# Kernel optimization log

Measured on AMD Instinct MI355X. Metric: run time of the kernel, lower is better.

Reference implementation:

```python
import jax, jax.numpy as jnp
import numpy as np

S, B, R, H, TOP, CHL = 512, 32, 8, 128, 3, 19
I = CHL + 1  # GRU input size after null-channel concat


def setup_inputs() -> dict:
    key = jax.random.key(0)
    ks = jax.random.split(key, 12)
    f = lambda k, shp, sc=0.05: jax.random.normal(k, shp, dtype=jnp.float32) * sc
    return {
        "x": f(ks[0], (B, CHL, S), 1.0),
        "Wih": f(ks[1], (R, 3 * H, I)),      # per-rim GRU input weights (torch order r,z,n)
        "Whh": f(ks[2], (R, 3 * H, H)),      # per-rim GRU hidden weights
        "Qir_w": f(ks[3], (H, H)),
        "Qir_b": f(ks[4], (H,)),
        "Kir_w": f(ks[5], (H, S)),
        "Vir_w": f(ks[6], (H, S)),
        "Qrr_w": f(ks[7], (H, H)),
        "Krr_w": f(ks[8], (H, H)),
        "Vrr_w": f(ks[9], (H, H)),
    }


def reference(x, Wih, Whh, Qir_w, Qir_b, Kir_w, Vir_w, Qrr_w, Krr_w, Vrr_w):
    Bn = x.shape[0]
    # prepend null channel, reshape to (S, B, I)
    xc = jnp.concatenate([jnp.zeros((Bn, 1, x.shape[2]), x.dtype), x], axis=1)
    xs = jnp.transpose(xc, (2, 0, 1))  # (S, B, I)

    # ---- per-rim GRU (no bias), torch gate order (r, z, n) ----
    x_proj = jnp.einsum('sbi,rgi->srbg', xs, Wih)  # (S, R, B, 3H)

    def step(hprev, xp):
        hp = jnp.einsum('rbh,rgh->rbg', hprev, Whh)
        xr, xz, xn = jnp.split(xp, 3, axis=-1)
        hr, hz, hn = jnp.split(hp, 3, axis=-1)
        r = jax.nn.sigmoid(xr + hr)
        z = jax.nn.sigmoid(xz + hz)
        n = jnp.tanh(xn + r * hn)
        hnew = (1.0 - z) * n + z * hprev
        return hnew, hnew

    h0 = jnp.zeros((R, Bn, H), x.dtype)
    _, hs = jax.lax.scan(step, h0, x_proj)      # (S, R, B, H)
    h = jnp.transpose(hs, (1, 0, 2, 3))          # (R, S, B, H)

    # ---- stage one: input attention + rim competition ----
    x_bis = jnp.transpose(xs, (1, 2, 0))         # (B, I, S)
    q = jnp.einsum('rsbh,oh->rsbo', h, Qir_w) + Qir_b
    k = jnp.einsum('bis,os->bio', x_bis, Kir_w)
    v = jnp.einsum('bis,os->bio', x_bis, Vir_w)
    qk = jnp.einsum('rsbh,bih->sbri', q, k) / (H ** 0.5)
    soft = jax.nn.softmax(qk, axis=3)            # (S, B, R, I)
    idx = jax.lax.top_k(-soft[..., 0], TOP)[1]   # (S, B, TOP)
    mask = jnp.sum(jax.nn.one_hot(idx, R, dtype=jnp.float32), axis=-2)[..., None]  # (S,B,R,1)
    mask = jax.lax.stop_gradient(mask)
    qkv = jnp.einsum('sbri,bih->sbrh', soft, v)  # (S, B, R, H)

    # NoGrad: forward identity, backward grad*mask
    h1 = qkv * mask + jax.lax.stop_gradient(qkv * (1.0 - mask))

    # ---- stage two: rim-rim attention, masked ----
    q2 = jnp.einsum('sbrh,oh->sbro', h1, Qrr_w)
    k2 = jnp.einsum('sbrh,oh->sbro', h1, Krr_w)
    v2 = jnp.einsum('sbrh,oh->sbro', h1, Vrr_w)
    qk2 = jnp.einsum('sbrh,sbch->sbrc', q2, k2)  # (S, B, R, R), no scaling (as in source)
    soft2 = jax.nn.softmax(qk2, axis=3) * mask
    out = h1 + jnp.einsum('sbrc,sbch->sbrh', soft2, v2)
    return out * mask
```

## Files before the change

### kernel.cpp

```cpp
#include <hip/hip_runtime.h>
#include <math.h>


typedef float v2f __attribute__((ext_vector_type(2)));
__device__ __forceinline__ v2f pkfma(v2f a, v2f b, v2f c) {
    return __builtin_elementwise_fma(a, b, c);
}

__global__ void kT(const float* __restrict__ Kir, const float* __restrict__ Vir,
                   const float* __restrict__ Vrr,
                   float* __restrict__ KirT, float* __restrict__ VirT,
                   float* __restrict__ VrrT) {
    int idx = blockIdx.x * 256 + threadIdx.x;
    if (idx < 65536) {
        int s = idx >> 7, o = idx & 127;
        KirT[idx] = Kir[o * 512 + s];
    } else if (idx < 131072) {
        int j = idx - 65536;
        int s = j >> 7, o = j & 127;
        VirT[j] = Vir[o * 512 + s];
    } else if (idx < 147456) {
        int j = idx - 131072;
        int g = j >> 7, h = j & 127;
        VrrT[j] = Vrr[h * 128 + g];
    }
}

__global__ __launch_bounds__(128) void kKV(const float* __restrict__ x,
        const float* __restrict__ KirT, const float* __restrict__ VirT,
        float* __restrict__ kbuf, float* __restrict__ vbuf) {
    const int b = blockIdx.x / 20, i = blockIdx.x % 20;
    const int o = threadIdx.x;
    if (i == 0) {
        kbuf[(b * 20) * 128 + o] = 0.0f;
        vbuf[(b * 20) * 128 + o] = 0.0f;
        return;
    }
    __shared__ float xL[512];
    for (int idx = threadIdx.x; idx < 512; idx += 128)
        xL[idx] = x[(b * 19 + (i - 1)) * 512 + idx];
    __syncthreads();
    float ak = 0.0f, av = 0.0f;
#pragma unroll 4
    for (int s = 0; s < 512; ++s) {
        float xv = xL[s];
        ak += xv * KirT[s * 128 + o];
        av += xv * VirT[s * 128 + o];
    }
    kbuf[(b * 20 + i) * 128 + o] = ak;
    vbuf[(b * 20 + i) * 128 + o] = av;
}

__global__ __launch_bounds__(128) void kKQ(const float* __restrict__ kbuf,
        const float* __restrict__ Qir, const float* __restrict__ Qib,
        float* __restrict__ KQ, float* __restrict__ cb) {
    const int b = blockIdx.x / 20, i = blockIdx.x % 20;
    const int h = threadIdx.x;
    __shared__ float kL[128];
    kL[h] = kbuf[(b * 20 + i) * 128 + h];
    __syncthreads();
    float acc = 0.0f;
#pragma unroll 4
    for (int o = 0; o < 128; ++o) acc += kL[o] * Qir[o * 128 + h];
    KQ[(b * 20 + i) * 128 + h] = acc;
    if (h == 0) {
        float c = 0.0f;
        for (int o = 0; o < 128; ++o) c += kL[o] * Qib[o];
        cb[b * 20 + i] = c;
    }
}

__global__ __launch_bounds__(256) void kM(const float* __restrict__ Qrr,
        const float* __restrict__ Krr, float* __restrict__ M) {
    const int h = blockIdx.x * 2 + (threadIdx.x >> 7);
    const int g = threadIdx.x & 127;
    float acc = 0.0f;
#pragma unroll 4
    for (int o = 0; o < 128; ++o) acc += Qrr[o * 128 + h] * Krr[o * 128 + g];
    M[h * 128 + g] = acc;
}

template<int CTRL>
__device__ __forceinline__ float dppadd(float v) {
    int r = __builtin_amdgcn_update_dpp(0, __float_as_int(v), CTRL, 0xF, 0xF, true);
    return v + __int_as_float(r);
}

__global__ __launch_bounds__(512, 2) void kGRU(const float* __restrict__ x,
        const float* __restrict__ Wih, const float* __restrict__ Whh,
        float* __restrict__ hs) {
    const int r = blockIdx.x >> 5;
    const int b = blockIdx.x & 31;
    const int t = threadIdx.x;
    const int j = t >> 2;
    const int kq = t & 3;

    __shared__ __align__(16) float xT[512 * 20];
    __shared__ __align__(16) float hsBuf[64 * 144];

    for (int idx = t; idx < 19 * 512; idx += 512) {
        int c = idx >> 9, s = idx & 511;
        xT[s * 20 + c] = x[(b * 19 + c) * 512 + s];
    }
    if (t < 144) hsBuf[63 * 144 + t] = 0.0f;

    v2f w0[16], w1[16], w2[16];
    {
        const float* Wb = Whh + (r * 384) * 128 + kq * 32;
        const float4* s0p = (const float4*)(Wb + (j) * 128);
        const float4* s1p = (const float4*)(Wb + (j + 128) * 128);
        const float4* s2p = (const float4*)(Wb + (j + 256) * 128);
#pragma unroll
        for (int u = 0; u < 8; ++u) {
            float4 a = s0p[u];
            w0[2*u]   = (v2f){a.x, a.y};
            w0[2*u+1] = (v2f){a.z, a.w};
            float4 bb = s1p[u];
            w1[2*u]   = (v2f){bb.x, bb.y};
            w1[2*u+1] = (v2f){bb.z, bb.w};
            float4 cc = s2p[u];
            w2[2*u]   = (v2f){cc.x, cc.y};
            w2[2*u+1] = (v2f){cc.z, cc.w};
        }
    }
    v2f wiv[9];
    float wlast;
    if (kq < 3) {
        const float* W = Wih + (r * 384 + (j + 128 * kq)) * 20;
#pragma unroll
        for (int c = 0; c < 9; ++c) wiv[c] = (v2f){W[2*c + 1], W[2*c + 2]};
        wlast = W[19];
    } else {
#pragma unroll
        for (int c = 0; c < 9; ++c) wiv[c] = (v2f){0.0f, 0.0f};
        wlast = 0.0f;
    }
    __syncthreads();

    const int jmap = j + ((j >> 5) << 2);
    const int cellBase = (b * 8 + r) * 128;
    float hprev = 0.0f;

    for (int s = 0; s < 512; ++s) {
        const int rowR = (s + 63) & 63;
        const float4* hp4 = (const float4*)(hsBuf + rowR * 144 + kq * 36);
        float4 hv[8];
#pragma unroll
        for (int u = 0; u < 8; ++u) hv[u] = hp4[u];

        v2f a0 = {0.0f, 0.0f}, a1 = {0.0f, 0.0f}, a2 = {0.0f, 0.0f};
#pragma unroll
        for (int u = 0; u < 8; ++u) {
            float4 h4 = hv[u];
            v2f hl = (v2f){h4.x, h4.y};
            v2f hh = (v2f){h4.z, h4.w};
            a0 = pkfma(w0[2*u], hl, a0); a0 = pkfma(w0[2*u+1], hh, a0);
            a1 = pkfma(w1[2*u], hl, a1); a1 = pkfma(w1[2*u+1], hh, a1);
            a2 = pkfma(w2[2*u], hl, a2); a2 = pkfma(w2[2*u+1], hh, a2);
        }
        float p0 = a0.x + a0.y;
        float p1 = a1.x + a1.y;
        float p2 = a2.x + a2.y;

        float xp;
        {
            const float4* xp4 = (const float4*)(xT + s * 20);
            float4 xa = xp4[0], xb = xp4[1], xc = xp4[2], xd = xp4[3], xe = xp4[4];
            v2f xacc = {0.0f, 0.0f};
            xacc = pkfma(wiv[0], (v2f){xa.x, xa.y}, xacc);
            xacc = pkfma(wiv[1], (v2f){xa.z, xa.w}, xacc);
            xacc = pkfma(wiv[2], (v2f){xb.x, xb.y}, xacc);
            xacc = pkfma(wiv[3], (v2f){xb.z, xb.w}, xacc);
            xacc = pkfma(wiv[4], (v2f){xc.x, xc.y}, xacc);
            xacc = pkfma(wiv[5], (v2f){xc.z, xc.w}, xacc);
            xacc = pkfma(wiv[6], (v2f){xd.x, xd.y}, xacc);
            xacc = pkfma(wiv[7], (v2f){xd.z, xd.w}, xacc);
            xacc = pkfma(wiv[8], (v2f){xe.x, xe.y}, xacc);
            xp = xacc.x + xacc.y + wlast * xe.z;
        }
        p0 += (kq == 0) ? xp : 0.0f;
        p1 += (kq == 1) ? xp : 0.0f;
        float p3 = (kq == 2) ? xp : 0.0f;

        p0 = dppadd<0xB1>(p0); p0 = dppadd<0x4E>(p0);
        p1 = dppadd<0xB1>(p1); p1 = dppadd<0x4E>(p1);
        p2 = dppadd<0xB1>(p2); p2 = dppadd<0x4E>(p2);
        p3 = dppadd<0xB1>(p3); p3 = dppadd<0x4E>(p3);

        float rg = __builtin_amdgcn_rcpf(1.0f + __expf(-p0));
        float zg = __builtin_amdgcn_rcpf(1.0f + __expf(-p1));
        float a  = p3 + rg * p2;
        float ng = 1.0f - 2.0f * __builtin_amdgcn_rcpf(__expf(2.0f * a) + 1.0f);
        float hnew = ng + zg * (hprev - ng);
        hprev = hnew;
        if (kq == 0) hsBuf[(s & 63) * 144 + jmap] = hnew;
        __syncthreads();

        if ((s & 63) == 63) {
            const int sBase = s - 63;
            const int c4 = (t & 31) * 4;
            const int cm = c4 + ((c4 >> 5) << 2);
#pragma unroll
            for (int w = 0; w < 4; ++w) {
                int rr = (t >> 5) + w * 16;
                float4 v = *(const float4*)(hsBuf + rr * 144 + cm);
                *(float4*)(hs + (size_t)(sBase + rr) * 32768 + cellBase + c4) = v;
            }
            __syncthreads();
        }
    }
}

__global__ __launch_bounds__(256) void kS1(const float* __restrict__ hs,
        const float* __restrict__ KQ, const float* __restrict__ cb,
        const float* __restrict__ vbuf,
        float* __restrict__ h1, int* __restrict__ widx, float* __restrict__ out) {
    const int b = blockIdx.x & 31;
    const int s0 = (blockIdx.x >> 5) * 16;
    const int t = threadIdx.x;
    __shared__ float KQL[20 * 132];
    __shared__ float vL[20 * 128];
    __shared__ float cbL[20];
    __shared__ float hLt[8 * 132];
    __shared__ float qkL[8 * 20];
    __shared__ float sfL[8 * 20];
    __shared__ float s0L[8];
    __shared__ int wselL[3];

    for (int idx = t; idx < 2560; idx += 256) {
        int i = idx >> 7, h = idx & 127;
        KQL[i * 132 + h] = KQ[(b * 20 + i) * 128 + h];
        vL[i * 128 + h] = vbuf[(b * 20 + i) * 128 + h];
    }
    if (t < 20) cbL[t] = cb[b * 20 + t];
    __syncthreads();

    for (int p = 0; p < 16; ++p) {
        const int s = s0 + p;
        for (int idx = t; idx < 1024; idx += 256) {
            int r = idx >> 7, h = idx & 127;
            hLt[r * 132 + h] = hs[((s * 32 + b) * 8 + r) * 128 + h];
        }
        __syncthreads();
        if (t < 152) {
            int r = t / 19, i = t % 19 + 1;
            const float* hr = &hLt[r * 132];
            const float* kg = &KQL[i * 132];
            float a = 0.0f;
#pragma unroll 4
            for (int h = 0; h < 128; ++h) a += hr[h] * kg[h];
            qkL[r * 20 + i] = (a + cbL[i]) * 0.08838834764831845f;
        }
        if (t < 8) qkL[t * 20] = 0.0f;
        __syncthreads();
        if (t < 8) {
            float m = -3.4e38f;
            for (int i = 0; i < 20; ++i) m = fmaxf(m, qkL[t * 20 + i]);
            float sum = 0.0f;
            for (int i = 0; i < 20; ++i) {
                float e = expf(qkL[t * 20 + i] - m);
                sfL[t * 20 + i] = e;
                sum += e;
            }
            float inv = 1.0f / sum;
            for (int i = 0; i < 20; ++i) sfL[t * 20 + i] *= inv;
            s0L[t] = sfL[t * 20];
        }
        __syncthreads();
        if (t == 0) {
            unsigned chosen = 0;
            for (int n = 0; n < 3; ++n) {
                float best = 3.4e38f; int bi = 0;
                for (int r2 = 0; r2 < 8; ++r2) {
                    if (chosen & (1u << r2)) continue;
                    float v = s0L[r2];
                    if (v < best) { best = v; bi = r2; }
                }
                chosen |= (1u << bi);
                wselL[n] = bi;
                widx[(s * 32 + b) * 3 + n] = bi;
            }
        }
        __syncthreads();
        {
            const int h = t & 127, rq = t >> 7;
            float a0 = 0, a1 = 0, a2 = 0, a3 = 0;
            for (int i = 1; i < 20; ++i) {
                float vv = vL[i * 128 + h];
                a0 += sfL[(rq * 4 + 0) * 20 + i] * vv;
                a1 += sfL[(rq * 4 + 1) * 20 + i] * vv;
                a2 += sfL[(rq * 4 + 2) * 20 + i] * vv;
                a3 += sfL[(rq * 4 + 3) * 20 + i] * vv;
            }
            const int pairBase = (s * 32 + b) * 8;
            float av[4] = {a0, a1, a2, a3};
#pragma unroll
            for (int jj = 0; jj < 4; ++jj) {
                int rim = rq * 4 + jj;
                h1[(pairBase + rim) * 128 + h] = av[jj];
                bool win = (wselL[0] == rim) || (wselL[1] == rim) || (wselL[2] == rim);
                if (!win) out[(pairBase + rim) * 128 + h] = 0.0f;
            }
        }
        __syncthreads();
    }
}

template<int EPI>
__global__ __launch_bounds__(256) void kGemm(
        const float* __restrict__ Asrc,
        const float* __restrict__ Bm,
        const int* __restrict__ widx,
        const float* __restrict__ h1g,
        float* __restrict__ C) {
    __shared__ float ALt[64][132];
    __shared__ float BL[64][128];
    const int n0 = blockIdx.x * 128;
    const int t = threadIdx.x;
    const int tr = t >> 4, tc = t & 15;
    const int q0 = 2 * tc, q1 = 2 * tc + 1;
    const int bq0 = (q0 ^ (q0 >> 3)) * 4;
    const int bq1 = (q1 ^ (q1 >> 3)) * 4;
    float acc[8][8];
#pragma unroll
    for (int i = 0; i < 8; ++i)
#pragma unroll
        for (int jj = 0; jj < 8; ++jj) acc[i][jj] = 0.0f;

    for (int kc = 0; kc < 128; kc += 64) {
        __syncthreads();
#pragma unroll
        for (int i = 0; i < 8; ++i) {
            int idx = t + i * 256;
            int row = idx >> 4, qk = idx & 15;
            const float* src;
            if (EPI == 0) {
                int n = n0 + row;
                int pair = n / 3;
                int rim = widx[n];
                src = Asrc + ((pair << 3) + rim) * 128 + kc + qk * 4;
            } else {
                src = Asrc + (n0 + row) * 128 + kc + qk * 4;
            }
            float4 a = *(const float4*)src;
            ALt[qk * 4 + 0][row] = a.x;
            ALt[qk * 4 + 1][row] = a.y;
            ALt[qk * 4 + 2][row] = a.z;
            ALt[qk * 4 + 3][row] = a.w;
        }
#pragma unroll
        for (int i = 0; i < 8; ++i) {
            int idx = t + i * 256;
            int kk = idx >> 5, qc = idx & 31;
            float4 bv = *(const float4*)(Bm + (kc + kk) * 128 + qc * 4);
            int pos = (qc ^ (qc >> 3)) * 4;
            *(float4*)&BL[kk][pos] = bv;
        }
        __syncthreads();
#pragma unroll 2
        for (int k = 0; k < 64; ++k) {
            float4 a0 = *(const float4*)&ALt[k][8 * tr];
            float4 a1 = *(const float4*)&ALt[k][8 * tr + 4];
            float4 b0 = *(const float4*)&BL[k][bq0];
            float4 b1 = *(const float4*)&BL[k][bq1];
            float ar[8] = {a0.x, a0.y, a0.z, a0.w, a1.x, a1.y, a1.z, a1.w};
            float bc[8] = {b0.x, b0.y, b0.z, b0.w, b1.x, b1.y, b1.z, b1.w};
#pragma unroll
            for (int i = 0; i < 8; ++i)
#pragma unroll
                for (int jj = 0; jj < 8; ++jj) acc[i][jj] += ar[i] * bc[jj];
        }
    }
    if (EPI == 0) {
#pragma unroll
        for (int i = 0; i < 8; ++i) {
            int row = n0 + 8 * tr + i;
            *(float4*)(C + row * 128 + 8 * tc) =
                make_float4(acc[i][0], acc[i][1], acc[i][2], acc[i][3]);
            *(float4*)(C + row * 128 + 8 * tc + 4) =
                make_float4(acc[i][4], acc[i][5], acc[i][6], acc[i][7]);
        }
    } else {
#pragma unroll
        for (int i = 0; i < 8; ++i) {
            int n = n0 + 8 * tr + i;
            int pair = n / 3;
            int rim = widx[n];
            int base = ((pair << 3) + rim) * 128 + 8 * tc;
            float4 w0 = *(const float4*)(h1g + base);
            float4 w1 = *(const float4*)(h1g + base + 4);
            *(float4*)(C + base) = make_float4(acc[i][0] + w0.x, acc[i][1] + w0.y,
                                               acc[i][2] + w0.z, acc[i][3] + w0.w);
            *(float4*)(C + base + 4) = make_float4(acc[i][4] + w1.x, acc[i][5] + w1.y,
                                                   acc[i][6] + w1.z, acc[i][7] + w1.w);
        }
    }
}

__global__ __launch_bounds__(256) void kS2c(const float* __restrict__ T1,
        const float* __restrict__ h1, float* __restrict__ U) {
    const int w = threadIdx.x >> 6;
    const int lane = threadIdx.x & 63;
    const int p = blockIdx.x * 4 + w;
    const int base8 = p * 8 * 128;
    float hv0[8], hv1[8];
#pragma unroll
    for (int c = 0; c < 8; ++c) {
        hv0[c] = h1[base8 + c * 128 + lane];
        hv1[c] = h1[base8 + c * 128 + 64 + lane];
    }
    float t0[3], t1v[3];
#pragma unroll
    for (int wr = 0; wr < 3; ++wr) {
        t0[wr]  = T1[(p * 3 + wr) * 128 + lane];
        t1v[wr] = T1[(p * 3 + wr) * 128 + 64 + lane];
    }
    float pr[3][8];
#pragma unroll
    for (int wr = 0; wr < 3; ++wr)
#pragma unroll
        for (int c = 0; c < 8; ++c)
            pr[wr][c] = t0[wr] * hv0[c] + t1v[wr] * hv1[c];
#pragma unroll
    for (int off = 32; off > 0; off >>= 1)
#pragma unroll
        for (int wr = 0; wr < 3; ++wr)
#pragma unroll
            for (int c = 0; c < 8; ++c)
                pr[wr][c] += __shfl_xor(pr[wr][c], off, 64);
#pragma unroll
    for (int wr = 0; wr < 3; ++wr) {
        float m = pr[wr][0];
#pragma unroll
        for (int c = 1; c < 8; ++c) m = fmaxf(m, pr[wr][c]);
        float sum = 0.0f;
#pragma unroll
        for (int c = 0; c < 8; ++c) { pr[wr][c] = expf(pr[wr][c] - m); sum += pr[wr][c]; }
        float inv = 1.0f / sum;
        float u0 = 0.0f, u1 = 0.0f;
#pragma unroll
        for (int c = 0; c < 8; ++c) {
            float sv = pr[wr][c] * inv;
            u0 += sv * hv0[c];
            u1 += sv * hv1[c];
        }
        U[(p * 3 + wr) * 128 + lane] = u0;
        U[(p * 3 + wr) * 128 + 64 + lane] = u1;
    }
}

extern "C" void kernel_launch(void* const* d_in, const int* in_sizes, int n_in,
                              void* d_out, int out_size, void* d_ws, size_t ws_size,
                              hipStream_t stream) {
    const float* x   = (const float*)d_in[0];
    const float* Wih = (const float*)d_in[1];
    const float* Whh = (const float*)d_in[2];
    const float* Qir = (const float*)d_in[3];
    const float* Qib = (const float*)d_in[4];
    const float* Kir = (const float*)d_in[5];
    const float* Vir = (const float*)d_in[6];
    const float* Qrr = (const float*)d_in[7];
    const float* Krr = (const float*)d_in[8];
    const float* Vrr = (const float*)d_in[9];
    float* out = (float*)d_out;
    float* ws  = (float*)d_ws;

    float* hs   = ws;
    float* h1   = ws + 16777216;
    float* KirT = ws + 33554432;
    float* VirT = ws + 33619968;
    float* VrrT = ws + 33685504;
    float* kb   = ws + 33701888;
    float* vb   = ws + 33783808;
    float* KQ   = ws + 33865728;
    float* cb   = ws + 33947648;
    float* Mm   = ws + 33948288;
    int*   widx = (int*)(ws + 33964672);
    float* T1   = ws;
    float* U    = ws + 6291456;

    (void)in_sizes; (void)n_in; (void)out_size; (void)ws_size;

    kT  <<<576, 256, 0, stream>>>(Kir, Vir, Vrr, KirT, VirT, VrrT);
    kKV <<<640, 128, 0, stream>>>(x, KirT, VirT, kb, vb);
    kKQ <<<640, 128, 0, stream>>>(kb, Qir, Qib, KQ, cb);
    kM  <<<64, 256, 0, stream>>>(Qrr, Krr, Mm);
    kGRU<<<256, 512, 0, stream>>>(x, Wih, Whh, hs);
    kS1 <<<1024, 256, 0, stream>>>(hs, KQ, cb, vb, h1, widx, out);
    kGemm<0><<<384, 256, 0, stream>>>(h1, Mm, widx, nullptr, T1);
    kS2c<<<4096, 256, 0, stream>>>(T1, h1, U);
    kGemm<1><<<384, 256, 0, stream>>>(U, VrrT, widx, h1, out);
}
```

Before: 570.4 us.

## Split GRU hidden-state dot products across eight lanes with 1024-thread blocks

The recurrent GRU kernel now spreads each hidden unit's Whh dot product over 8 lanes instead of 4 and launches 1024 threads per block. This halves each lane's serial packed-FMA chain and its register weight footprint per timestep, which should shorten the latency-bound 512-step recurrence. The cost is one extra DPP reduction step (row_half_mirror) per gate. The block barrier per step also has to synchronise twice as many waves. The shared hidden-state buffer is re-padded (20 floats per 16) to match the new 8-way read pattern, and the write-back is rewritten for it.

```diff
diff --git a/kernel.cpp b/kernel.cpp
--- a/kernel.cpp
+++ b/kernel.cpp
@@ -86,32 +86,32 @@
     return v + __int_as_float(r);
 }
 
-__global__ __launch_bounds__(512, 2) void kGRU(const float* __restrict__ x,
+__global__ __launch_bounds__(1024) void kGRU(const float* __restrict__ x,
         const float* __restrict__ Wih, const float* __restrict__ Whh,
         float* __restrict__ hs) {
     const int r = blockIdx.x >> 5;
     const int b = blockIdx.x & 31;
     const int t = threadIdx.x;
-    const int j = t >> 2;
-    const int kq = t & 3;
+    const int j = t >> 3;
+    const int kq = t & 7;
 
     __shared__ __align__(16) float xT[512 * 20];
-    __shared__ __align__(16) float hsBuf[64 * 144];
-
-    for (int idx = t; idx < 19 * 512; idx += 512) {
+    __shared__ __align__(16) float hsBuf[64 * 160];
+
+    for (int idx = t; idx < 19 * 512; idx += 1024) {
         int c = idx >> 9, s = idx & 511;
         xT[s * 20 + c] = x[(b * 19 + c) * 512 + s];
     }
-    if (t < 144) hsBuf[63 * 144 + t] = 0.0f;
-
-    v2f w0[16], w1[16], w2[16];
+    if (t < 160) hsBuf[63 * 160 + t] = 0.0f;
+
+    v2f w0[8], w1[8], w2[8];
     {
-        const float* Wb = Whh + (r * 384) * 128 + kq * 32;
+        const float* Wb = Whh + (r * 384) * 128 + kq * 16;
         const float4* s0p = (const float4*)(Wb + (j) * 128);
         const float4* s1p = (const float4*)(Wb + (j + 128) * 128);
         const float4* s2p = (const float4*)(Wb + (j + 256) * 128);
 #pragma unroll
-        for (int u = 0; u < 8; ++u) {
+        for (int u = 0; u < 4; ++u) {
             float4 a = s0p[u];
             w0[2*u]   = (v2f){a.x, a.y};
             w0[2*u+1] = (v2f){a.z, a.w};
@@ -137,27 +137,29 @@
     }
     __syncthreads();
 
-    const int jmap = j + ((j >> 5) << 2);
+    const int hoff = kq * 20;
+    const int jw = (j >> 4) * 20 + (j & 15);
     const int cellBase = (b * 8 + r) * 128;
     float hprev = 0.0f;
 
     for (int s = 0; s < 512; ++s) {
         const int rowR = (s + 63) & 63;
-        const float4* hp4 = (const float4*)(hsBuf + rowR * 144 + kq * 36);
-        float4 hv[8];
-#pragma unroll
-        for (int u = 0; u < 8; ++u) hv[u] = hp4[u];
+        const float4* hp4 = (const float4*)(hsBuf + rowR * 160 + hoff);
+        float4 h0 = hp4[0], h1v = hp4[1], h2 = hp4[2], h3 = hp4[3];
 
         v2f a0 = {0.0f, 0.0f}, a1 = {0.0f, 0.0f}, a2 = {0.0f, 0.0f};
-#pragma unroll
-        for (int u = 0; u < 8; ++u) {
-            float4 h4 = hv[u];
-            v2f hl = (v2f){h4.x, h4.y};
-            v2f hh = (v2f){h4.z, h4.w};
-            a0 = pkfma(w0[2*u], hl, a0); a0 = pkfma(w0[2*u+1], hh, a0);
-            a1 = pkfma(w1[2*u], hl, a1); a1 = pkfma(w1[2*u+1], hh, a1);
-            a2 = pkfma(w2[2*u], hl, a2); a2 = pkfma(w2[2*u+1], hh, a2);
-        }
+        v2f hh0 = (v2f){h0.x, h0.y}, hh1 = (v2f){h0.z, h0.w};
+        v2f hh2 = (v2f){h1v.x, h1v.y}, hh3 = (v2f){h1v.z, h1v.w};
+        v2f hh4 = (v2f){h2.x, h2.y}, hh5 = (v2f){h2.z, h2.w};
+        v2f hh6 = (v2f){h3.x, h3.y}, hh7 = (v2f){h3.z, h3.w};
+        a0 = pkfma(w0[0], hh0, a0); a1 = pkfma(w1[0], hh0, a1); a2 = pkfma(w2[0], hh0, a2);
+        a0 = pkfma(w0[1], hh1, a0); a1 = pkfma(w1[1], hh1, a1); a2 = pkfma(w2[1], hh1, a2);
+        a0 = pkfma(w0[2], hh2, a0); a1 = pkfma(w1[2], hh2, a1); a2 = pkfma(w2[2], hh2, a2);
+        a0 = pkfma(w0[3], hh3, a0); a1 = pkfma(w1[3], hh3, a1); a2 = pkfma(w2[3], hh3, a2);
+        a0 = pkfma(w0[4], hh4, a0); a1 = pkfma(w1[4], hh4, a1); a2 = pkfma(w2[4], hh4, a2);
+        a0 = pkfma(w0[5], hh5, a0); a1 = pkfma(w1[5], hh5, a1); a2 = pkfma(w2[5], hh5, a2);
+        a0 = pkfma(w0[6], hh6, a0); a1 = pkfma(w1[6], hh6, a1); a2 = pkfma(w2[6], hh6, a2);
+        a0 = pkfma(w0[7], hh7, a0); a1 = pkfma(w1[7], hh7, a1); a2 = pkfma(w2[7], hh7, a2);
         float p0 = a0.x + a0.y;
         float p1 = a1.x + a1.y;
         float p2 = a2.x + a2.y;
@@ -182,10 +184,10 @@
         p1 += (kq == 1) ? xp : 0.0f;
         float p3 = (kq == 2) ? xp : 0.0f;
 
-        p0 = dppadd<0xB1>(p0); p0 = dppadd<0x4E>(p0);
-        p1 = dppadd<0xB1>(p1); p1 = dppadd<0x4E>(p1);
-        p2 = dppadd<0xB1>(p2); p2 = dppadd<0x4E>(p2);
-        p3 = dppadd<0xB1>(p3); p3 = dppadd<0x4E>(p3);
+        p0 = dppadd<0xB1>(p0); p0 = dppadd<0x4E>(p0); p0 = dppadd<0x141>(p0);
+        p1 = dppadd<0xB1>(p1); p1 = dppadd<0x4E>(p1); p1 = dppadd<0x141>(p1);
+        p2 = dppadd<0xB1>(p2); p2 = dppadd<0x4E>(p2); p2 = dppadd<0x141>(p2);
+        p3 = dppadd<0xB1>(p3); p3 = dppadd<0x4E>(p3); p3 = dppadd<0x141>(p3);
 
         float rg = __builtin_amdgcn_rcpf(1.0f + __expf(-p0));
         float zg = __builtin_amdgcn_rcpf(1.0f + __expf(-p1));
@@ -193,19 +195,18 @@
         float ng = 1.0f - 2.0f * __builtin_amdgcn_rcpf(__expf(2.0f * a) + 1.0f);
         float hnew = ng + zg * (hprev - ng);
         hprev = hnew;
-        if (kq == 0) hsBuf[(s & 63) * 144 + jmap] = hnew;
+        if (kq == 0) hsBuf[(s & 63) * 160 + jw] = hnew;
         __syncthreads();
 
         if ((s & 63) == 63) {
             const int sBase = s - 63;
-            const int c4 = (t & 31) * 4;
-            const int cm = c4 + ((c4 >> 5) << 2);
-#pragma unroll
-            for (int w = 0; w < 4; ++w) {
-                int rr = (t >> 5) + w * 16;
-                float4 v = *(const float4*)(hsBuf + rr * 144 + cm);
-                *(float4*)(hs + (size_t)(sBase + rr) * 32768 + cellBase + c4) = v;
-            }
+            const int fr = t >> 4;
+            const int c0 = (t & 15) * 8;
+            const int lo = (c0 >> 4) * 20 + (c0 & 15);
+            float4 v0 = *(const float4*)(hsBuf + fr * 160 + lo);
+            float4 v1 = *(const float4*)(hsBuf + fr * 160 + lo + 4);
+            float4* dst = (float4*)(hs + (size_t)(sBase + fr) * 32768 + cellBase + c0);
+            dst[0] = v0; dst[1] = v1;
             __syncthreads();
         }
     }
@@ -485,7 +486,7 @@
     kKV <<<640, 128, 0, stream>>>(x, KirT, VirT, kb, vb);
     kKQ <<<640, 128, 0, stream>>>(kb, Qir, Qib, KQ, cb);
     kM  <<<64, 256, 0, stream>>>(Qrr, Krr, Mm);
-    kGRU<<<256, 512, 0, stream>>>(x, Wih, Whh, hs);
+    kGRU<<<256, 1024, 0, stream>>>(x, Wih, Whh, hs);
     kS1 <<<1024, 256, 0, stream>>>(hs, KQ, cb, vb, h1, widx, out);
     kGemm<0><<<384, 256, 0, stream>>>(h1, Mm, widx, nullptr, T1);
     kS2c<<<4096, 256, 0, stream>>>(T1, h1, U);
```

Result: slower. 668.2 us (+17.1%).
